# Optimization experiments

Measured on AMD Instinct MI355X. Metric: run time of the kernel, lower is better.

The kernel has to match this reference:

```python
import jax, jax.numpy as jnp
import numpy as np

B, T, D_IN, H, OUT = 512, 512, 64, 256, 64
EPS = 1e-5


def _ln(x, w, b):
    m = x.mean(-1, keepdims=True)
    v = ((x - m) ** 2).mean(-1, keepdims=True)
    return (x - m) / jnp.sqrt(v + EPS) * w + b


def _cell(x, h_prev, Wg, bg, gnw, gnb, Wc, bc, cnw, cnb):
    # LayerNormGRU cell
    combined = jnp.concatenate([x, h_prev], axis=-1)          # [B, D+H]
    rz = _ln(combined @ Wg.T + bg, gnw, gnb)                  # [B, 2H]
    r, z = jnp.split(rz, 2, axis=-1)
    r, z = jax.nn.sigmoid(r), jax.nn.sigmoid(z)
    combined_r = jnp.concatenate([x, r * h_prev], axis=-1)
    n = jnp.tanh(_ln(combined_r @ Wc.T + bc, cnw, cnb))       # [B, H]
    return (1.0 - z) * h_prev + z * n


def setup_inputs() -> dict:
    key = jax.random.key(0)
    ks = jax.random.split(key, 24)

    def uni(k, shape, fan_in):
        lim = 1.0 / np.sqrt(fan_in)
        return jax.random.uniform(k, shape, jnp.float32, -lim, lim)

    d0 = D_IN + H   # layer 0 cell input width
    d1 = H + H      # layer 1 cell input width
    return {
        "x": jax.random.normal(ks[0], (B, T, D_IN), jnp.float32),
        # layer 0
        "Wg0": uni(ks[1], (2 * H, d0), d0), "bg0": uni(ks[2], (2 * H,), d0),
        "gnw0": jnp.ones((2 * H,), jnp.float32), "gnb0": jnp.zeros((2 * H,), jnp.float32),
        "Wc0": uni(ks[3], (H, d0), d0), "bc0": uni(ks[4], (H,), d0),
        "cnw0": jnp.ones((H,), jnp.float32), "cnb0": jnp.zeros((H,), jnp.float32),
        # layer 1
        "Wg1": uni(ks[5], (2 * H, d1), d1), "bg1": uni(ks[6], (2 * H,), d1),
        "gnw1": jnp.ones((2 * H,), jnp.float32), "gnb1": jnp.zeros((2 * H,), jnp.float32),
        "Wc1": uni(ks[7], (H, d1), d1), "bc1": uni(ks[8], (H,), d1),
        "cnw1": jnp.ones((H,), jnp.float32), "cnb1": jnp.zeros((H,), jnp.float32),
        # output head
        "fcW": uni(ks[9], (OUT, H), H), "fcb": uni(ks[10], (OUT,), H),
    }


def reference(x, Wg0, bg0, gnw0, gnb0, Wc0, bc0, cnw0, cnb0,
              Wg1, bg1, gnw1, gnb1, Wc1, bc1, cnw1, cnb1, fcW, fcb):
    b = x.shape[0]
    h_init = (jnp.zeros((b, H), x.dtype), jnp.zeros((b, H), x.dtype))

    def step(carry, xt):
        h0, h1 = carry
        h0 = _cell(xt, h0, Wg0, bg0, gnw0, gnb0, Wc0, bc0, cnw0, cnb0)
        h1 = _cell(h0, h1, Wg1, bg1, gnw1, gnb1, Wc1, bc1, cnw1, cnb1)
        return (h0, h1), None

    (h0, h1), _ = jax.lax.scan(step, h_init, jnp.swapaxes(x, 0, 1))  # scan over T
    return h1 @ fcW.T + fcb  # [B, OUT]
```

## Files before the change

### kernel.cpp

```cpp
#include <hip/hip_runtime.h>


#define B_   512
#define T_   512
#define DIN  64
#define H_   256
#define OUT_ 64
#define EPS_ 1e-5f

typedef __attribute__((ext_vector_type(8))) short bf16x8;
typedef __attribute__((ext_vector_type(4))) float f32x4;

__device__ __forceinline__ unsigned short f2bf(float f) {
  unsigned int u = __float_as_uint(f);
  u += 0x7fffu + ((u >> 16) & 1u);
  return (unsigned short)(u >> 16);
}
__device__ __forceinline__ float bfh(unsigned short u) {
  return __uint_as_float(((unsigned int)u) << 16);
}
__device__ __forceinline__ float sigm_(float x) {
  return __builtin_amdgcn_rcpf(1.f + __expf(-x));
}
__device__ __forceinline__ float tanh_(float x) {
  return 1.f - 2.f * __builtin_amdgcn_rcpf(__expf(2.f * x) + 1.f);
}
template<int C>
__device__ __forceinline__ float dpp_add(float v) {
  int r = __builtin_amdgcn_update_dpp(0, __float_as_int(v), C, 0xF, 0xF, false);
  return v + __int_as_float(r);
}
__device__ __forceinline__ float red16(float v) {
  v = dpp_add<0x121>(v);
  v = dpp_add<0x122>(v);
  v = dpp_add<0x124>(v);
  v = dpp_add<0x128>(v);
  return v;
}

#define PIN8A(a) asm volatile("" : "+a"(a[0]), "+a"(a[1]), "+a"(a[2]), "+a"(a[3]), \
                                   "+a"(a[4]), "+a"(a[5]), "+a"(a[6]), "+a"(a[7]))

__global__ void prep_frag(const float* __restrict__ w, unsigned short* __restrict__ dst,
                          int N, int Ksrc, int koff) {
  int gid = blockIdx.x * 256 + threadIdx.x;
  if (gid >= N * 256) return;
  int n = gid >> 8, k = gid & 255;
  int idx = (((n >> 4) * 8 + (k >> 5)) * 64 + ((n & 15) + 16 * ((k >> 3) & 3))) * 8 + (k & 7);
  dst[idx] = f2bf(w[(size_t)n * Ksrc + koff + k]);
}

__global__ void prep_wx(const float* __restrict__ wg, const float* __restrict__ wc,
                        unsigned short* __restrict__ dst, int KX, int Kg, int Kc) {
  int gid = blockIdx.x * 256 + threadIdx.x;
  if (gid >= 768 * KX) return;
  int n = gid / KX, k = gid - n * KX;
  float v = (n < 512) ? wg[(size_t)n * Kg + k] : wc[(size_t)(n - 512) * Kc + k];
  dst[gid] = f2bf(v);
}

__global__ void bias_cat(const float* __restrict__ bg, const float* __restrict__ bc,
                         float* __restrict__ dst) {
  int i = blockIdx.x * 256 + threadIdx.x;
  if (i < 768) dst[i] = (i < 512) ? bg[i] : bc[i - 512];
}

template<int KX, bool AFP32>
__launch_bounds__(256)
__global__ void precomp(const void* __restrict__ Asrc,
                        const unsigned short* __restrict__ wx,
                        const float* __restrict__ bias,
                        unsigned short* __restrict__ Pc,
                        int TC, int t0)
{
  __shared__ __align__(16) unsigned short A_s[8 * 2 * 64 * 8];
  __shared__ __align__(16) unsigned short B_s[8 * 2 * 64 * 8];

  const int tid = threadIdx.x, lane = tid & 63, wv = tid >> 6;
  const int m0 = blockIdx.x * 128, nb = blockIdx.y * 128;
  const int bt = m0 / (TC * 16);
  const int tt0 = (m0 - bt * TC * 16) >> 4;
  const int mq = wv >> 1, nq = wv & 1;
  const int crow0 = (lane >> 4) * 4;

  f32x4 acc[4][4];
#pragma unroll
  for (int i = 0; i < 4; ++i)
#pragma unroll
    for (int j = 0; j < 4; ++j) acc[i][j] = (f32x4){0, 0, 0, 0};

  for (int kb = 0; kb < KX / 64; ++kb) {
    __syncthreads();
#pragma unroll
    for (int it = 0; it < 4; ++it) {
      int s = tid + it * 256;
      int rg = s >> 3, k8 = s & 7;
      int mt = rg >> 4, r15 = rg & 15;
      int dl = r15 + 16 * (k8 & 3), kc = k8 >> 2;
      if (AFP32) {
        const float* xp = (const float*)Asrc +
            (((size_t)(bt * 16 + r15)) * T_ + (t0 + tt0 + mt)) * DIN + kb * 64 + k8 * 8;
        float4 u0 = *(const float4*)xp, u1 = *(const float4*)(xp + 4);
        unsigned short tmp[8];
        tmp[0] = f2bf(u0.x); tmp[1] = f2bf(u0.y); tmp[2] = f2bf(u0.z); tmp[3] = f2bf(u0.w);
        tmp[4] = f2bf(u1.x); tmp[5] = f2bf(u1.y); tmp[6] = f2bf(u1.z); tmp[7] = f2bf(u1.w);
        *reinterpret_cast<bf16x8*>(&A_s[((mt * 2 + kc) * 64 + dl) * 8]) =
            *reinterpret_cast<bf16x8*>(tmp);
      } else {
        const unsigned short* ap = (const unsigned short*)Asrc +
            ((size_t)(m0 + rg)) * KX + kb * 64 + k8 * 8;
        *reinterpret_cast<bf16x8*>(&A_s[((mt * 2 + kc) * 64 + dl) * 8]) =
            *reinterpret_cast<const bf16x8*>(ap);
      }
      const unsigned short* bp = wx + ((size_t)(nb + rg)) * KX + kb * 64 + k8 * 8;
      *reinterpret_cast<bf16x8*>(&B_s[((mt * 2 + kc) * 64 + dl) * 8]) =
          *reinterpret_cast<const bf16x8*>(bp);
    }
    __syncthreads();
#pragma unroll
    for (int kc = 0; kc < 2; ++kc) {
      bf16x8 av[4], bv[4];
#pragma unroll
      for (int i = 0; i < 4; ++i) {
        av[i] = *reinterpret_cast<const bf16x8*>(&A_s[(((mq * 4 + i) * 2 + kc) * 64 + lane) * 8]);
        bv[i] = *reinterpret_cast<const bf16x8*>(&B_s[(((nq * 4 + i) * 2 + kc) * 64 + lane) * 8]);
      }
#pragma unroll
      for (int i = 0; i < 4; ++i)
#pragma unroll
        for (int j = 0; j < 4; ++j)
          acc[i][j] = __builtin_amdgcn_mfma_f32_16x16x32_bf16(av[i], bv[j], acc[i][j], 0, 0, 0);
    }
  }
  float bb[4];
#pragma unroll
  for (int j = 0; j < 4; ++j) bb[j] = bias[nb + nq * 64 + j * 16 + (lane & 15)];
#pragma unroll
  for (int i = 0; i < 4; ++i) {
    int tt = tt0 + mq * 4 + i;
#pragma unroll
    for (int j = 0; j < 4; ++j) {
      int n = nb + nq * 64 + j * 16 + (lane & 15);
      ushort4 o;
      o.x = f2bf(acc[i][j][0] + bb[j]); o.y = f2bf(acc[i][j][1] + bb[j]);
      o.z = f2bf(acc[i][j][2] + bb[j]); o.w = f2bf(acc[i][j][3] + bb[j]);
      *reinterpret_cast<ushort4*>(&Pc[((size_t)(bt * TC + tt) * 768 + n) * 16 + crow0]) = o;
    }
  }
}

__launch_bounds__(512, 2)
__global__ void gru_fused(
    const unsigned short* __restrict__ g0, const unsigned short* __restrict__ c0,
    const unsigned short* __restrict__ P0,
    const float* __restrict__ gnw0, const float* __restrict__ gnb0,
    const float* __restrict__ cnw0, const float* __restrict__ cnb0,
    float* __restrict__ hst0, unsigned short* __restrict__ h0out,
    const unsigned short* __restrict__ g1, const unsigned short* __restrict__ c1,
    const unsigned short* __restrict__ P1,
    const float* __restrict__ gnw1, const float* __restrict__ gnb1,
    const float* __restrict__ cnw1, const float* __restrict__ cnb1,
    float* __restrict__ hst1,
    int bActive, int dActive, int bFirst, int dFirst, int TC)
{
  __shared__ __align__(16) unsigned short wc_s[16 * 8 * 64 * 8];
  __shared__ __align__(16) unsigned short h_s[16][264];
  __shared__ __align__(16) unsigned short rh_s[16][264];
  __shared__ __align__(16) float sumP[8][20];
  __shared__ __align__(16) float sqP[8][20];
  __shared__ __align__(8) float2 mnrs[16];

  const bool isB = ((int)blockIdx.x) < 32;
  if (isB ? !bActive : !dActive) return;

  const unsigned short* gfrag = isB ? g0 : g1;
  const unsigned short* cfrag = isB ? c0 : c1;
  const unsigned short* Pc    = isB ? P0 : P1;
  const float* gnw = isB ? gnw0 : gnw1;
  const float* gnb = isB ? gnb0 : gnb1;
  const float* cnw = isB ? cnw0 : cnw1;
  const float* cnb = isB ? cnb0 : cnb1;
  float* hstate = isB ? hst0 : hst1;
  unsigned short* h0o = isB ? h0out : (unsigned short*)nullptr;
  const int first = isB ? bFirst : dFirst;
  const int bt = isB ? blockIdx.x : (blockIdx.x - 32);

  const int tid = threadIdx.x, lane = tid & 63, wv = tid >> 6;
  const int b0 = bt * 16;
  const int arow = lane & 15, koff = (lane >> 4) * 8, crow0 = (lane >> 4) * 4;
  const int colr0 = 32 * wv + (lane & 15), colr1 = colr0 + 16;
  const int nt0 = 2 * wv, nt1 = 2 * wv + 1, nt2 = 16 + 2 * wv, nt3 = 17 + 2 * wv;

  for (int i = tid; i < 8192; i += 512)
    *reinterpret_cast<bf16x8*>(&wc_s[i * 8]) = *reinterpret_cast<const bf16x8*>(&cfrag[i * 8]);

  bf16x8 wgr0[8], wgr1[8], wgr2[8], wgr3[8];
#pragma unroll
  for (int kc = 0; kc < 8; ++kc) {
    wgr0[kc] = *reinterpret_cast<const bf16x8*>(&gfrag[((nt0 * 8 + kc) * 64 + lane) * 8]);
    wgr1[kc] = *reinterpret_cast<const bf16x8*>(&gfrag[((nt1 * 8 + kc) * 64 + lane) * 8]);
    wgr2[kc] = *reinterpret_cast<const bf16x8*>(&gfrag[((nt2 * 8 + kc) * 64 + lane) * 8]);
    wgr3[kc] = *reinterpret_cast<const bf16x8*>(&gfrag[((nt3 * 8 + kc) * 64 + lane) * 8]);
  }

  const float gw_r0 = gnw[colr0], gb_r0 = gnb[colr0];
  const float gw_r1 = gnw[colr1], gb_r1 = gnb[colr1];
  const float gw_z0 = gnw[256 + colr0], gb_z0 = gnb[256 + colr0];
  const float gw_z1 = gnw[256 + colr1], gb_z1 = gnb[256 + colr1];
  const float cw0 = cnw[colr0], cb0 = cnb[colr0];
  const float cw1 = cnw[colr1], cb1 = cnb[colr1];

  float hm[2][4];
  if (first) {
#pragma unroll
    for (int g = 0; g < 4; ++g) { hm[0][g] = 0.f; hm[1][g] = 0.f; }
    for (int i = tid; i < 16 * 264; i += 512) (&h_s[0][0])[i] = 0;
  } else {
#pragma unroll
    for (int g = 0; g < 4; ++g) {
      hm[0][g] = hstate[(size_t)(b0 + crow0 + g) * 256 + colr0];
      hm[1][g] = hstate[(size_t)(b0 + crow0 + g) * 256 + colr1];
    }
    int r = tid >> 5, c8 = (tid & 31) * 8;
    float4 v0 = *reinterpret_cast<const float4*>(&hstate[(size_t)(b0 + r) * 256 + c8]);
    float4 v1 = *reinterpret_cast<const float4*>(&hstate[(size_t)(b0 + r) * 256 + c8 + 4]);
    ushort4 o0, o1;
    o0.x = f2bf(v0.x); o0.y = f2bf(v0.y); o0.z = f2bf(v0.z); o0.w = f2bf(v0.w);
    o1.x = f2bf(v1.x); o1.y = f2bf(v1.y); o1.z = f2bf(v1.z); o1.w = f2bf(v1.w);
    *reinterpret_cast<ushort4*>(&h_s[r][c8]) = o0;
    *reinterpret_cast<ushort4*>(&h_s[r][c8 + 4]) = o1;
  }
  __syncthreads();

  const unsigned short* Pr0 = Pc + ((size_t)bt * TC * 768 + colr0) * 16;

  for (int tt = 0; tt < TC; ++tt) {
    PIN8A(wgr0); PIN8A(wgr1); PIN8A(wgr2); PIN8A(wgr3);

    ushort4 pr0 = *reinterpret_cast<const ushort4*>(Pr0 + crow0);
    ushort4 pr1 = *reinterpret_cast<const ushort4*>(Pr0 + 16 * 16 + crow0);
    ushort4 pz0 = *reinterpret_cast<const ushort4*>(Pr0 + 256 * 16 + crow0);
    ushort4 pz1 = *reinterpret_cast<const ushort4*>(Pr0 + 272 * 16 + crow0);
    ushort4 pn0 = *reinterpret_cast<const ushort4*>(Pr0 + 512 * 16 + crow0);
    ushort4 pn1 = *reinterpret_cast<const ushort4*>(Pr0 + 528 * 16 + crow0);
    Pr0 += 12288;

    f32x4 a0 = {0, 0, 0, 0}, a1 = {0, 0, 0, 0}, a2 = {0, 0, 0, 0}, a3 = {0, 0, 0, 0};
#pragma unroll
    for (int kc = 0; kc < 8; ++kc) {
      bf16x8 av = *reinterpret_cast<const bf16x8*>(&h_s[arow][kc * 32 + koff]);
      a0 = __builtin_amdgcn_mfma_f32_16x16x32_bf16(av, wgr0[kc], a0, 0, 0, 0);
      a1 = __builtin_amdgcn_mfma_f32_16x16x32_bf16(av, wgr1[kc], a1, 0, 0, 0);
      a2 = __builtin_amdgcn_mfma_f32_16x16x32_bf16(av, wgr2[kc], a2, 0, 0, 0);
      a3 = __builtin_amdgcn_mfma_f32_16x16x32_bf16(av, wgr3[kc], a3, 0, 0, 0);
    }
    float vr0[4], vr1[4], vz0[4], vz1[4];
    {
      float s4[4], q4[4];
#pragma unroll
      for (int g = 0; g < 4; ++g) {
        vr0[g] = a0[g] + bfh(((const unsigned short*)&pr0)[g]);
        vr1[g] = a1[g] + bfh(((const unsigned short*)&pr1)[g]);
        vz0[g] = a2[g] + bfh(((const unsigned short*)&pz0)[g]);
        vz1[g] = a3[g] + bfh(((const unsigned short*)&pz1)[g]);
        s4[g] = red16(vr0[g] + vr1[g] + vz0[g] + vz1[g]);
        q4[g] = red16(vr0[g] * vr0[g] + vr1[g] * vr1[g] + vz0[g] * vz0[g] + vz1[g] * vz1[g]);
      }
      if ((lane & 15) == 0) {
        *reinterpret_cast<f32x4*>(&sumP[wv][crow0]) = (f32x4){s4[0], s4[1], s4[2], s4[3]};
        *reinterpret_cast<f32x4*>(&sqP[wv][crow0])  = (f32x4){q4[0], q4[1], q4[2], q4[3]};
      }
    }
    __syncthreads();

    {
      int sg = lane >> 4, rr = lane & 15;
      float S = sumP[2 * sg][rr] + sumP[2 * sg + 1][rr];
      float Q = sqP[2 * sg][rr] + sqP[2 * sg + 1][rr];
      S += __shfl_xor(S, 16, 64); Q += __shfl_xor(Q, 16, 64);
      S += __shfl_xor(S, 32, 64); Q += __shfl_xor(Q, 32, 64);
      float mn = S * (1.f / 512.f);
      float rs = __builtin_amdgcn_rsqf(Q * (1.f / 512.f) - mn * mn + EPS_);
      if (lane < 16) mnrs[lane] = make_float2(mn, rs);
    }
    float zf[2][4];
#pragma unroll
    for (int g = 0; g < 4; ++g) {
      float2 mr = mnrs[crow0 + g];
      float rv0 = sigm_(fmaf((vr0[g] - mr.x) * mr.y, gw_r0, gb_r0));
      float rv1 = sigm_(fmaf((vr1[g] - mr.x) * mr.y, gw_r1, gb_r1));
      zf[0][g]  = sigm_(fmaf((vz0[g] - mr.x) * mr.y, gw_z0, gb_z0));
      zf[1][g]  = sigm_(fmaf((vz1[g] - mr.x) * mr.y, gw_z1, gb_z1));
      rh_s[crow0 + g][colr0] = f2bf(rv0 * hm[0][g]);
      rh_s[crow0 + g][colr1] = f2bf(rv1 * hm[1][g]);
    }
    __syncthreads();

    f32x4 c0a = {0, 0, 0, 0}, c1a = {0, 0, 0, 0};
#pragma unroll
    for (int kc = 0; kc < 8; ++kc) {
      bf16x8 av = *reinterpret_cast<const bf16x8*>(&rh_s[arow][kc * 32 + koff]);
      bf16x8 b0v = *reinterpret_cast<const bf16x8*>(&wc_s[((nt0 * 8 + kc) * 64 + lane) * 8]);
      bf16x8 b1v = *reinterpret_cast<const bf16x8*>(&wc_s[((nt1 * 8 + kc) * 64 + lane) * 8]);
      c0a = __builtin_amdgcn_mfma_f32_16x16x32_bf16(av, b0v, c0a, 0, 0, 0);
      c1a = __builtin_amdgcn_mfma_f32_16x16x32_bf16(av, b1v, c1a, 0, 0, 0);
    }
    float vc0[4], vc1[4];
    {
      float s4[4], q4[4];
#pragma unroll
      for (int g = 0; g < 4; ++g) {
        vc0[g] = c0a[g] + bfh(((const unsigned short*)&pn0)[g]);
        vc1[g] = c1a[g] + bfh(((const unsigned short*)&pn1)[g]);
        s4[g] = red16(vc0[g] + vc1[g]);
        q4[g] = red16(vc0[g] * vc0[g] + vc1[g] * vc1[g]);
      }
      if ((lane & 15) == 0) {
        *reinterpret_cast<f32x4*>(&sumP[wv][crow0]) = (f32x4){s4[0], s4[1], s4[2], s4[3]};
        *reinterpret_cast<f32x4*>(&sqP[wv][crow0])  = (f32x4){q4[0], q4[1], q4[2], q4[3]};
      }
    }
    __syncthreads();

    {
      int sg = lane >> 4, rr = lane & 15;
      float S = sumP[2 * sg][rr] + sumP[2 * sg + 1][rr];
      float Q = sqP[2 * sg][rr] + sqP[2 * sg + 1][rr];
      S += __shfl_xor(S, 16, 64); Q += __shfl_xor(Q, 16, 64);
      S += __shfl_xor(S, 32, 64); Q += __shfl_xor(Q, 32, 64);
      float mn = S * (1.f / 256.f);
      float rs = __builtin_amdgcn_rsqf(Q * (1.f / 256.f) - mn * mn + EPS_);
      if (lane < 16) mnrs[lane] = make_float2(mn, rs);
    }
    unsigned short* hrow = h0o ? (h0o + (size_t)(bt * TC + tt) * 4096) : (unsigned short*)nullptr;
#pragma unroll
    for (int g = 0; g < 4; ++g) {
      float2 mr = mnrs[crow0 + g];
      float n0 = tanh_(fmaf((vc0[g] - mr.x) * mr.y, cw0, cb0));
      float n1 = tanh_(fmaf((vc1[g] - mr.x) * mr.y, cw1, cb1));
      float h0n = fmaf(zf[0][g], n0 - hm[0][g], hm[0][g]);
      float h1n = fmaf(zf[1][g], n1 - hm[1][g], hm[1][g]);
      hm[0][g] = h0n; hm[1][g] = h1n;
      unsigned short hb0 = f2bf(h0n), hb1 = f2bf(h1n);
      h_s[crow0 + g][colr0] = hb0;
      h_s[crow0 + g][colr1] = hb1;
      if (hrow) {
        hrow[(size_t)(crow0 + g) * 256 + colr0] = hb0;
        hrow[(size_t)(crow0 + g) * 256 + colr1] = hb1;
      }
    }
    __syncthreads();
  }

#pragma unroll
  for (int g = 0; g < 4; ++g) {
    hstate[(size_t)(b0 + crow0 + g) * 256 + colr0] = hm[0][g];
    hstate[(size_t)(b0 + crow0 + g) * 256 + colr1] = hm[1][g];
  }
}

__launch_bounds__(256)
__global__ void head_k(const float* __restrict__ h1, const float* __restrict__ fcW,
                       const float* __restrict__ fcb, float* __restrict__ out) {
  __shared__ float hs[16][256];
  const int tid = threadIdx.x, b0 = blockIdx.x * 16;
  for (int i = tid; i < 16 * 64; i += 256) {
    int r = i >> 6, c4 = (i & 63) * 4;
    *reinterpret_cast<float4*>(&hs[r][c4]) =
        *reinterpret_cast<const float4*>(&h1[(size_t)(b0 + r) * 256 + c4]);
  }
  __syncthreads();
  int r = tid >> 4, o = (tid & 15) * 4;
  float a0 = fcb[o], a1 = fcb[o + 1], a2 = fcb[o + 2], a3 = fcb[o + 3];
  for (int k = 0; k < 256; ++k) {
    float h = hs[r][k];
    a0 = fmaf(h, fcW[(size_t)(o + 0) * 256 + k], a0);
    a1 = fmaf(h, fcW[(size_t)(o + 1) * 256 + k], a1);
    a2 = fmaf(h, fcW[(size_t)(o + 2) * 256 + k], a2);
    a3 = fmaf(h, fcW[(size_t)(o + 3) * 256 + k], a3);
  }
  float4 ov = {a0, a1, a2, a3};
  *reinterpret_cast<float4*>(&out[(size_t)(b0 + r) * 64 + o]) = ov;
}

extern "C" void kernel_launch(void* const* d_in, const int* in_sizes, int n_in,
                              void* d_out, int out_size, void* d_ws, size_t ws_size,
                              hipStream_t stream) {
  (void)in_sizes; (void)n_in; (void)out_size;
  const float* x    = (const float*)d_in[0];
  const float* Wg0  = (const float*)d_in[1];
  const float* bg0  = (const float*)d_in[2];
  const float* gnw0 = (const float*)d_in[3];
  const float* gnb0 = (const float*)d_in[4];
  const float* Wc0  = (const float*)d_in[5];
  const float* bc0  = (const float*)d_in[6];
  const float* cnw0 = (const float*)d_in[7];
  const float* cnb0 = (const float*)d_in[8];
  const float* Wg1  = (const float*)d_in[9];
  const float* bg1  = (const float*)d_in[10];
  const float* gnw1 = (const float*)d_in[11];
  const float* gnb1 = (const float*)d_in[12];
  const float* Wc1  = (const float*)d_in[13];
  const float* bc1  = (const float*)d_in[14];
  const float* cnw1 = (const float*)d_in[15];
  const float* cnb1 = (const float*)d_in[16];
  const float* fcW  = (const float*)d_in[17];
  const float* fcb  = (const float*)d_in[18];

  float* hst0 = (float*)d_ws;
  float* hst1 = hst0 + 131072;
  float* b768_0 = hst1 + 131072;
  float* b768_1 = b768_0 + 768;
  unsigned short* g0h = (unsigned short*)(b768_1 + 768);
  unsigned short* c0h = g0h + 131072;
  unsigned short* g1h = c0h + 65536;
  unsigned short* c1h = g1h + 131072;
  unsigned short* wx0 = c1h + 65536;
  unsigned short* wx1 = wx0 + 49152;
  unsigned short* dynbase = wx1 + 196608;

  const size_t fixed_bytes = (size_t)((char*)dynbase - (char*)d_ws);
  int TC = 64;
  while (TC > 8) {
    size_t need = fixed_bytes + (size_t)TC * (262144 + 2 * 786432);
    if (need <= ws_size) break;
    TC >>= 1;
  }
  const int NC = T_ / TC;

  unsigned short* P0c = dynbase;
  unsigned short* P1c = P0c + (size_t)TC * 393216;
  unsigned short* h0c = P1c + (size_t)TC * 393216;

  prep_frag<<<512, 256, 0, stream>>>(Wg0, g0h, 512, 320, 64);
  prep_frag<<<256, 256, 0, stream>>>(Wc0, c0h, 256, 320, 64);
  prep_frag<<<512, 256, 0, stream>>>(Wg1, g1h, 512, 512, 256);
  prep_frag<<<256, 256, 0, stream>>>(Wc1, c1h, 256, 512, 256);
  prep_wx<<<192, 256, 0, stream>>>(Wg0, Wc0, wx0, 64, 320, 320);
  prep_wx<<<768, 256, 0, stream>>>(Wg1, Wc1, wx1, 256, 512, 512);
  bias_cat<<<3, 256, 0, stream>>>(bg0, bc0, b768_0);
  bias_cat<<<3, 256, 0, stream>>>(bg1, bc1, b768_1);

  dim3 pgrid(4 * TC, 6);

  precomp<64, true><<<pgrid, 256, 0, stream>>>(x, wx0, b768_0, P0c, TC, 0);
  gru_fused<<<32, 512, 0, stream>>>(
      g0h, c0h, P0c, gnw0, gnb0, cnw0, cnb0, hst0, h0c,
      g1h, c1h, P1c, gnw1, gnb1, cnw1, cnb1, hst1,
      1, 0, 1, 0, TC);
  precomp<256, false><<<pgrid, 256, 0, stream>>>(h0c, wx1, b768_1, P1c, TC, 0);
  if (NC > 1)
    precomp<64, true><<<pgrid, 256, 0, stream>>>(x, wx0, b768_0, P0c, TC, TC);

  for (int c = 0; c < NC; ++c) {
    int bAct = (c + 1 < NC) ? 1 : 0;
    gru_fused<<<64, 512, 0, stream>>>(
        g0h, c0h, P0c, gnw0, gnb0, cnw0, cnb0, hst0, h0c,
        g1h, c1h, P1c, gnw1, gnb1, cnw1, cnb1, hst1,
        bAct, 1, 0, (c == 0) ? 1 : 0, TC);
    if (c + 1 < NC)
      precomp<256, false><<<pgrid, 256, 0, stream>>>(h0c, wx1, b768_1, P1c, TC, 0);
    if (c + 2 < NC)
      precomp<64, true><<<pgrid, 256, 0, stream>>>(x, wx0, b768_0, P0c, TC, (c + 2) * TC);
  }

  head_k<<<32, 256, 0, stream>>>(hst1, fcW, fcb, (float*)d_out);
}
```

Before: 2.732 ms.

## Fuse recurrent and input-projection stages into one pipelined megakernel with double buffering

```diff
diff --git a/kernel.cpp b/kernel.cpp
--- a/kernel.cpp
+++ b/kernel.cpp
@@ -65,19 +65,14 @@
   if (i < 768) dst[i] = (i < 512) ? bg[i] : bc[i - 512];
 }
 
-template<int KX, bool AFP32>
-__launch_bounds__(256)
-__global__ void precomp(const void* __restrict__ Asrc,
-                        const unsigned short* __restrict__ wx,
-                        const float* __restrict__ bias,
-                        unsigned short* __restrict__ Pc,
-                        int TC, int t0)
+__device__ __forceinline__ void precomp_tile(
+    const void* __restrict__ Asrc, const unsigned short* __restrict__ wx,
+    const float* __restrict__ bias, unsigned short* __restrict__ Pc,
+    int TC, int t0, int KX, int AFP32,
+    int mi, int nb, unsigned short* A_s, unsigned short* B_s, int t256)
 {
-  __shared__ __align__(16) unsigned short A_s[8 * 2 * 64 * 8];
-  __shared__ __align__(16) unsigned short B_s[8 * 2 * 64 * 8];
-
-  const int tid = threadIdx.x, lane = tid & 63, wv = tid >> 6;
-  const int m0 = blockIdx.x * 128, nb = blockIdx.y * 128;
+  const int lane = t256 & 63, wv = t256 >> 6;
+  const int m0 = mi * 128;
   const int bt = m0 / (TC * 16);
   const int tt0 = (m0 - bt * TC * 16) >> 4;
   const int mq = wv >> 1, nq = wv & 1;
@@ -89,11 +84,11 @@
 #pragma unroll
     for (int j = 0; j < 4; ++j) acc[i][j] = (f32x4){0, 0, 0, 0};
 
-  for (int kb = 0; kb < KX / 64; ++kb) {
+  for (int kb = 0; kb < (KX >> 6); ++kb) {
     __syncthreads();
 #pragma unroll
     for (int it = 0; it < 4; ++it) {
-      int s = tid + it * 256;
+      int s = t256 + it * 256;
       int rg = s >> 3, k8 = s & 7;
       int mt = rg >> 4, r15 = rg & 15;
       int dl = r15 + 16 * (k8 & 3), kc = k8 >> 2;
@@ -149,41 +144,33 @@
   }
 }
 
-__launch_bounds__(512, 2)
-__global__ void gru_fused(
-    const unsigned short* __restrict__ g0, const unsigned short* __restrict__ c0,
-    const unsigned short* __restrict__ P0,
-    const float* __restrict__ gnw0, const float* __restrict__ gnb0,
-    const float* __restrict__ cnw0, const float* __restrict__ cnb0,
-    float* __restrict__ hst0, unsigned short* __restrict__ h0out,
-    const unsigned short* __restrict__ g1, const unsigned short* __restrict__ c1,
-    const unsigned short* __restrict__ P1,
-    const float* __restrict__ gnw1, const float* __restrict__ gnb1,
-    const float* __restrict__ cnw1, const float* __restrict__ cnb1,
-    float* __restrict__ hst1,
-    int bActive, int dActive, int bFirst, int dFirst, int TC)
+__launch_bounds__(256)
+__global__ void precomp_std(const void* __restrict__ Asrc,
+                            const unsigned short* __restrict__ wx,
+                            const float* __restrict__ bias,
+                            unsigned short* __restrict__ Pc,
+                            int TC, int t0, int KX, int AFP32) {
+  __shared__ __align__(16) unsigned short A_s[8192];
+  __shared__ __align__(16) unsigned short B_s[8192];
+  precomp_tile(Asrc, wx, bias, Pc, TC, t0, KX, AFP32,
+               blockIdx.x, blockIdx.y * 128, A_s, B_s, threadIdx.x);
+}
+
+__device__ __forceinline__ void gru_body(
+    unsigned char* smem, int bt,
+    const unsigned short* __restrict__ gfrag,
+    const unsigned short* __restrict__ cfrag,
+    const unsigned short* __restrict__ Pc,
+    const float* __restrict__ gnw, const float* __restrict__ gnb,
+    const float* __restrict__ cnw, const float* __restrict__ cnb,
+    float* __restrict__ hstate, unsigned short* __restrict__ h0out,
+    int TC, int first)
 {
-  __shared__ __align__(16) unsigned short wc_s[16 * 8 * 64 * 8];
-  __shared__ __align__(16) unsigned short h_s[16][264];
-  __shared__ __align__(16) unsigned short rh_s[16][264];
-  __shared__ __align__(16) float sumP[8][20];
-  __shared__ __align__(16) float sqP[8][20];
-  __shared__ __align__(8) float2 mnrs[16];
-
-  const bool isB = ((int)blockIdx.x) < 32;
-  if (isB ? !bActive : !dActive) return;
-
-  const unsigned short* gfrag = isB ? g0 : g1;
-  const unsigned short* cfrag = isB ? c0 : c1;
-  const unsigned short* Pc    = isB ? P0 : P1;
-  const float* gnw = isB ? gnw0 : gnw1;
-  const float* gnb = isB ? gnb0 : gnb1;
-  const float* cnw = isB ? cnw0 : cnw1;
-  const float* cnb = isB ? cnb0 : cnb1;
-  float* hstate = isB ? hst0 : hst1;
-  unsigned short* h0o = isB ? h0out : (unsigned short*)nullptr;
-  const int first = isB ? bFirst : dFirst;
-  const int bt = isB ? blockIdx.x : (blockIdx.x - 32);
+  unsigned short* wc_s = (unsigned short*)smem;
+  unsigned short (*h_s)[264]  = (unsigned short(*)[264])(smem + 131072);
+  unsigned short (*rh_s)[264] = (unsigned short(*)[264])(smem + 139520);
+  float (*sumP)[20] = (float(*)[20])(smem + 147968);
+  float (*sqP)[20]  = (float(*)[20])(smem + 148608);
 
   const int tid = threadIdx.x, lane = tid & 63, wv = tid >> 6;
   const int b0 = bt * 16;
@@ -232,18 +219,27 @@
   }
   __syncthreads();
 
-  const unsigned short* Pr0 = Pc + ((size_t)bt * TC * 768 + colr0) * 16;
+  const unsigned short* Pr = Pc + ((size_t)bt * TC * 768 + colr0) * 16;
+  ushort4 npr0 = *reinterpret_cast<const ushort4*>(Pr + crow0);
+  ushort4 npr1 = *reinterpret_cast<const ushort4*>(Pr + 256 + crow0);
+  ushort4 npz0 = *reinterpret_cast<const ushort4*>(Pr + 4096 + crow0);
+  ushort4 npz1 = *reinterpret_cast<const ushort4*>(Pr + 4352 + crow0);
+  ushort4 npn0 = *reinterpret_cast<const ushort4*>(Pr + 8192 + crow0);
+  ushort4 npn1 = *reinterpret_cast<const ushort4*>(Pr + 8448 + crow0);
 
   for (int tt = 0; tt < TC; ++tt) {
     PIN8A(wgr0); PIN8A(wgr1); PIN8A(wgr2); PIN8A(wgr3);
 
-    ushort4 pr0 = *reinterpret_cast<const ushort4*>(Pr0 + crow0);
-    ushort4 pr1 = *reinterpret_cast<const ushort4*>(Pr0 + 16 * 16 + crow0);
-    ushort4 pz0 = *reinterpret_cast<const ushort4*>(Pr0 + 256 * 16 + crow0);
-    ushort4 pz1 = *reinterpret_cast<const ushort4*>(Pr0 + 272 * 16 + crow0);
-    ushort4 pn0 = *reinterpret_cast<const ushort4*>(Pr0 + 512 * 16 + crow0);
-    ushort4 pn1 = *reinterpret_cast<const ushort4*>(Pr0 + 528 * 16 + crow0);
-    Pr0 += 12288;
+    ushort4 pr0 = npr0, pr1 = npr1, pz0 = npz0, pz1 = npz1, pn0 = npn0, pn1 = npn1;
+    if (tt + 1 < TC) {
+      Pr += 12288;
+      npr0 = *reinterpret_cast<const ushort4*>(Pr + crow0);
+      npr1 = *reinterpret_cast<const ushort4*>(Pr + 256 + crow0);
+      npz0 = *reinterpret_cast<const ushort4*>(Pr + 4096 + crow0);
+      npz1 = *reinterpret_cast<const ushort4*>(Pr + 4352 + crow0);
+      npn0 = *reinterpret_cast<const ushort4*>(Pr + 8192 + crow0);
+      npn1 = *reinterpret_cast<const ushort4*>(Pr + 8448 + crow0);
+    }
 
     f32x4 a0 = {0, 0, 0, 0}, a1 = {0, 0, 0, 0}, a2 = {0, 0, 0, 0}, a3 = {0, 0, 0, 0};
 #pragma unroll
@@ -273,6 +269,7 @@
     }
     __syncthreads();
 
+    float zf[2][4];
     {
       int sg = lane >> 4, rr = lane & 15;
       float S = sumP[2 * sg][rr] + sumP[2 * sg + 1][rr];
@@ -281,18 +278,17 @@
       S += __shfl_xor(S, 32, 64); Q += __shfl_xor(Q, 32, 64);
       float mn = S * (1.f / 512.f);
       float rs = __builtin_amdgcn_rsqf(Q * (1.f / 512.f) - mn * mn + EPS_);
-      if (lane < 16) mnrs[lane] = make_float2(mn, rs);
-    }
-    float zf[2][4];
-#pragma unroll
-    for (int g = 0; g < 4; ++g) {
-      float2 mr = mnrs[crow0 + g];
-      float rv0 = sigm_(fmaf((vr0[g] - mr.x) * mr.y, gw_r0, gb_r0));
-      float rv1 = sigm_(fmaf((vr1[g] - mr.x) * mr.y, gw_r1, gb_r1));
-      zf[0][g]  = sigm_(fmaf((vz0[g] - mr.x) * mr.y, gw_z0, gb_z0));
-      zf[1][g]  = sigm_(fmaf((vz1[g] - mr.x) * mr.y, gw_z1, gb_z1));
-      rh_s[crow0 + g][colr0] = f2bf(rv0 * hm[0][g]);
-      rh_s[crow0 + g][colr1] = f2bf(rv1 * hm[1][g]);
+#pragma unroll
+      for (int g = 0; g < 4; ++g) {
+        float m_ = __shfl(mn, crow0 + g, 64);
+        float r_ = __shfl(rs, crow0 + g, 64);
+        float rv0 = sigm_(fmaf((vr0[g] - m_) * r_, gw_r0, gb_r0));
+        float rv1 = sigm_(fmaf((vr1[g] - m_) * r_, gw_r1, gb_r1));
+        zf[0][g]  = sigm_(fmaf((vz0[g] - m_) * r_, gw_z0, gb_z0));
+        zf[1][g]  = sigm_(fmaf((vz1[g] - m_) * r_, gw_z1, gb_z1));
+        rh_s[crow0 + g][colr0] = f2bf(rv0 * hm[0][g]);
+        rh_s[crow0 + g][colr1] = f2bf(rv1 * hm[1][g]);
+      }
     }
     __syncthreads();
 
@@ -330,23 +326,23 @@
       S += __shfl_xor(S, 32, 64); Q += __shfl_xor(Q, 32, 64);
       float mn = S * (1.f / 256.f);
       float rs = __builtin_amdgcn_rsqf(Q * (1.f / 256.f) - mn * mn + EPS_);
-      if (lane < 16) mnrs[lane] = make_float2(mn, rs);
-    }
-    unsigned short* hrow = h0o ? (h0o + (size_t)(bt * TC + tt) * 4096) : (unsigned short*)nullptr;
-#pragma unroll
-    for (int g = 0; g < 4; ++g) {
-      float2 mr = mnrs[crow0 + g];
-      float n0 = tanh_(fmaf((vc0[g] - mr.x) * mr.y, cw0, cb0));
-      float n1 = tanh_(fmaf((vc1[g] - mr.x) * mr.y, cw1, cb1));
-      float h0n = fmaf(zf[0][g], n0 - hm[0][g], hm[0][g]);
-      float h1n = fmaf(zf[1][g], n1 - hm[1][g], hm[1][g]);
-      hm[0][g] = h0n; hm[1][g] = h1n;
-      unsigned short hb0 = f2bf(h0n), hb1 = f2bf(h1n);
-      h_s[crow0 + g][colr0] = hb0;
-      h_s[crow0 + g][colr1] = hb1;
-      if (hrow) {
-        hrow[(size_t)(crow0 + g) * 256 + colr0] = hb0;
-        hrow[(size_t)(crow0 + g) * 256 + colr1] = hb1;
+      unsigned short* hrow = h0out ? (h0out + (size_t)(bt * TC + tt) * 4096) : (unsigned short*)nullptr;
+#pragma unroll
+      for (int g = 0; g < 4; ++g) {
+        float m_ = __shfl(mn, crow0 + g, 64);
+        float r_ = __shfl(rs, crow0 + g, 64);
+        float n0 = tanh_(fmaf((vc0[g] - m_) * r_, cw0, cb0));
+        float n1 = tanh_(fmaf((vc1[g] - m_) * r_, cw1, cb1));
+        float h0n = fmaf(zf[0][g], n0 - hm[0][g], hm[0][g]);
+        float h1n = fmaf(zf[1][g], n1 - hm[1][g], hm[1][g]);
+        hm[0][g] = h0n; hm[1][g] = h1n;
+        unsigned short hb0 = f2bf(h0n), hb1 = f2bf(h1n);
+        h_s[crow0 + g][colr0] = hb0;
+        h_s[crow0 + g][colr1] = hb1;
+        if (hrow) {
+          hrow[(size_t)(crow0 + g) * 256 + colr0] = hb0;
+          hrow[(size_t)(crow0 + g) * 256 + colr1] = hb1;
+        }
       }
     }
     __syncthreads();
@@ -356,6 +352,67 @@
   for (int g = 0; g < 4; ++g) {
     hstate[(size_t)(b0 + crow0 + g) * 256 + colr0] = hm[0][g];
     hstate[(size_t)(b0 + crow0 + g) * 256 + colr1] = hm[1][g];
+  }
+}
+
+__launch_bounds__(512, 2)
+__global__ void mega(
+    const float* __restrict__ x,
+    const unsigned short* __restrict__ g0h, const unsigned short* __restrict__ c0h,
+    const unsigned short* __restrict__ g1h, const unsigned short* __restrict__ c1h,
+    const unsigned short* __restrict__ wx0, const unsigned short* __restrict__ wx1,
+    const float* __restrict__ b768_0, const float* __restrict__ b768_1,
+    const float* __restrict__ gnw0, const float* __restrict__ gnb0,
+    const float* __restrict__ cnw0, const float* __restrict__ cnb0,
+    const float* __restrict__ gnw1, const float* __restrict__ gnb1,
+    const float* __restrict__ cnw1, const float* __restrict__ cnb1,
+    float* __restrict__ hst0, float* __restrict__ hst1,
+    unsigned short* __restrict__ P0a, unsigned short* __restrict__ P0b,
+    unsigned short* __restrict__ P1a, unsigned short* __restrict__ P1b,
+    unsigned short* __restrict__ h0a, unsigned short* __restrict__ h0b,
+    int k, int TC, int NC)
+{
+  __shared__ __align__(16) unsigned char smem[149504];
+  const int bid = blockIdx.x;
+
+  if (bid < 32) {
+    if (k >= NC) return;
+    unsigned short* P0 = (k & 1) ? P0b : P0a;
+    unsigned short* h0 = (k & 1) ? h0b : h0a;
+    gru_body(smem, bid, g0h, c0h, P0, gnw0, gnb0, cnw0, cnb0, hst0, h0, TC, k == 0);
+  } else if (bid < 64) {
+    int kD = k - 2;
+    if (kD < 0 || kD >= NC) return;
+    unsigned short* P1 = (kD & 1) ? P1b : P1a;
+    gru_body(smem, bid - 32, g1h, c1h, P1, gnw1, gnb1, cnw1, cnb1, hst1,
+             (unsigned short*)nullptr, TC, kD == 0);
+  } else if (bid < 160) {
+    int kA = k + 1;
+    if (kA >= NC) return;
+    unsigned short* P0 = (kA & 1) ? P0b : P0a;
+    int team = (bid - 64) * 2 + (threadIdx.x >> 8);
+    int t256 = threadIdx.x & 255;
+    unsigned short* A_s = (unsigned short*)(smem + (threadIdx.x >> 8) * 32768);
+    unsigned short* B_s = A_s + 8192;
+    int ntile = 24 * TC;
+    for (int i = team; i < ntile; i += 192) {
+      int mi = i % (4 * TC), ni = i / (4 * TC);
+      precomp_tile(x, wx0, b768_0, P0, TC, kA * TC, 64, 1, mi, ni * 128, A_s, B_s, t256);
+    }
+  } else {
+    int kC = k - 1;
+    if (kC < 0 || kC >= NC) return;
+    const unsigned short* h0 = (kC & 1) ? h0b : h0a;
+    unsigned short* P1 = (kC & 1) ? P1b : P1a;
+    int team = (bid - 160) * 2 + (threadIdx.x >> 8);
+    int t256 = threadIdx.x & 255;
+    unsigned short* A_s = (unsigned short*)(smem + (threadIdx.x >> 8) * 32768);
+    unsigned short* B_s = A_s + 8192;
+    int ntile = 24 * TC;
+    for (int i = team; i < ntile; i += 192) {
+      int mi = i % (4 * TC), ni = i / (4 * TC);
+      precomp_tile(h0, wx1, b768_1, P1, TC, 0, 256, 0, mi, ni * 128, A_s, B_s, t256);
+    }
   }
 }
 
@@ -420,17 +477,20 @@
   unsigned short* dynbase = wx1 + 196608;
 
   const size_t fixed_bytes = (size_t)((char*)dynbase - (char*)d_ws);
-  int TC = 64;
-  while (TC > 8) {
-    size_t need = fixed_bytes + (size_t)TC * (262144 + 2 * 786432);
+  int TC = 32;
+  while (TC > 4) {
+    size_t need = fixed_bytes + (size_t)TC * 3670016;
     if (need <= ws_size) break;
     TC >>= 1;
   }
   const int NC = T_ / TC;
 
-  unsigned short* P0c = dynbase;
-  unsigned short* P1c = P0c + (size_t)TC * 393216;
-  unsigned short* h0c = P1c + (size_t)TC * 393216;
+  unsigned short* P0a = dynbase;
+  unsigned short* P0b = P0a + (size_t)TC * 393216;
+  unsigned short* P1a = P0b + (size_t)TC * 393216;
+  unsigned short* P1b = P1a + (size_t)TC * 393216;
+  unsigned short* h0a = P1b + (size_t)TC * 393216;
+  unsigned short* h0b = h0a + (size_t)TC * 131072;
 
   prep_frag<<<512, 256, 0, stream>>>(Wg0, g0h, 512, 320, 64);
   prep_frag<<<256, 256, 0, stream>>>(Wc0, c0h, 256, 320, 64);
@@ -441,27 +501,12 @@
   bias_cat<<<3, 256, 0, stream>>>(bg0, bc0, b768_0);
   bias_cat<<<3, 256, 0, stream>>>(bg1, bc1, b768_1);
 
-  dim3 pgrid(4 * TC, 6);
-
-  precomp<64, true><<<pgrid, 256, 0, stream>>>(x, wx0, b768_0, P0c, TC, 0);
-  gru_fused<<<32, 512, 0, stream>>>(
-      g0h, c0h, P0c, gnw0, gnb0, cnw0, cnb0, hst0, h0c,
-      g1h, c1h, P1c, gnw1, gnb1, cnw1, cnb1, hst1,
-      1, 0, 1, 0, TC);
-  precomp<256, false><<<pgrid, 256, 0, stream>>>(h0c, wx1, b768_1, P1c, TC, 0);
-  if (NC > 1)
-    precomp<64, true><<<pgrid, 256, 0, stream>>>(x, wx0, b768_0, P0c, TC, TC);
-
-  for (int c = 0; c < NC; ++c) {
-    int bAct = (c + 1 < NC) ? 1 : 0;
-    gru_fused<<<64, 512, 0, stream>>>(
-        g0h, c0h, P0c, gnw0, gnb0, cnw0, cnb0, hst0, h0c,
-        g1h, c1h, P1c, gnw1, gnb1, cnw1, cnb1, hst1,
-        bAct, 1, 0, (c == 0) ? 1 : 0, TC);
-    if (c + 1 < NC)
-      precomp<256, false><<<pgrid, 256, 0, stream>>>(h0c, wx1, b768_1, P1c, TC, 0);
-    if (c + 2 < NC)
-      precomp<64, true><<<pgrid, 256, 0, stream>>>(x, wx0, b768_0, P0c, TC, (c + 2) * TC);
+  precomp_std<<<dim3(4 * TC, 6), 256, 0, stream>>>(x, wx0, b768_0, P0a, TC, 0, 64, 1);
+
+  for (int k = 0; k < NC + 2; ++k) {
+    mega<<<256, 512, 0, stream>>>(x, g0h, c0h, g1h, c1h, wx0, wx1, b768_0, b768_1,
+        gnw0, gnb0, cnw0, cnb0, gnw1, gnb1, cnw1, cnb1,
+        hst0, hst1, P0a, P0b, P1a, P1b, h0a, h0b, k, TC, NC);
   }
 
   head_k<<<32, 256, 0, stream>>>(hst1, fcW, fcb, (float*)d_out);
```

Measured after the change: 2.630 ms (median of 2 runs). 3.7% less time.
